# Performance work log

Measured on AMD Instinct MI355X. Metric: run time of the kernel, lower is better.

The kernel has to match this reference:

```python
import jax, jax.numpy as jnp
import numpy as np

B = 2            # batch_size (number of windows)
W_SIZE = 2       # window_size
WIDTH = 256      # cart_pixel_width
TEMP = 0.01      # softmax_temp
EPS = 1e-12      # F.normalize eps


def _l2norm(x, axis):
    n = jnp.sqrt(jnp.sum(x * x, axis=axis, keepdims=True))
    return x / jnp.maximum(n, EPS)


def _bilinear(img, u, v):
    """align_corners=True bilinear sample. img: [C,H,W]; u,v: [N] pixel coords."""
    H, W = img.shape[-2], img.shape[-1]
    u0 = jnp.clip(jnp.floor(u), 0, W - 1)
    v0 = jnp.clip(jnp.floor(v), 0, H - 1)
    u1 = jnp.clip(u0 + 1, 0, W - 1)
    v1 = jnp.clip(v0 + 1, 0, H - 1)
    au = u - u0
    av = v - v0
    u0i, u1i = u0.astype(jnp.int32), u1.astype(jnp.int32)
    v0i, v1i = v0.astype(jnp.int32), v1.astype(jnp.int32)
    g = lambda vi, ui: img[:, vi, ui]  # [C,N]
    return (g(v0i, u0i) * (1 - au) * (1 - av) + g(v0i, u1i) * au * (1 - av)
            + g(v1i, u0i) * (1 - au) * av + g(v1i, u1i) * au * av)


def setup_inputs() -> dict:
    key = jax.random.key(0)
    k1, k2, k3, k4 = jax.random.split(key, 4)
    BW, C, N, S = B * W_SIZE, 248, 1024, 1
    return {
        "keypoint_scores": jax.random.normal(k1, (BW, S, N), dtype=jnp.float32),
        "keypoint_desc": jax.random.normal(k2, (BW, C, N), dtype=jnp.float32),
        "desc_dense": jax.random.normal(k3, (BW, C, WIDTH, WIDTH), dtype=jnp.float32),
        "times_img": jax.random.uniform(k4, (BW, 1, WIDTH, WIDTH), dtype=jnp.float32),
    }


def reference(keypoint_scores, keypoint_desc, desc_dense, times_img):
    BW, C, N = keypoint_desc.shape
    w = W_SIZE
    # frame index bookkeeping (same as the torch per-batch loop, vectorized)
    src_ids = jnp.arange(B) * w                                   # [B]
    tgt_ids = (jnp.arange(B)[:, None] * w
               + jnp.arange(1, w)[None, :]).reshape(-1)           # [B*(w-1)]

    # dense pixel coordinates [W^2, 2] in (u, v) order
    v, u = jnp.meshgrid(jnp.arange(WIDTH), jnp.arange(WIDTH), indexing='ij')
    coords = jnp.stack([u.reshape(-1), v.reshape(-1)], axis=1).astype(desc_dense.dtype)

    # normalized source dense descriptors [B, C, W^2]
    src = _l2norm(desc_dense[src_ids].reshape(B, C, -1), axis=1)
    # normalized target keypoint descriptors [B, w-1, C, N]
    tgt = _l2norm(keypoint_desc[tgt_ids].reshape(B, w - 1, C, N), axis=2)

    # dense correlation: [B, w-1, N, W^2]
    match_vals = jnp.einsum('bkcn,bcm->bknm', tgt, src)
    soft = jax.nn.softmax(match_vals / TEMP, axis=-1)
    # coordinate-weighted sum -> pseudo coords [B*(w-1), N, 2]
    pseudo_coords = jnp.einsum('bknm,md->bknd', soft, coords).reshape(B * (w - 1), N, 2)

    # bilinear-sample src times at pseudo coords (normalize->grid_sample round trip
    # with align_corners maps back to the same pixel coords; H == W here)
    src_times = jnp.repeat(times_img[src_ids], w - 1, axis=0)      # [B*(w-1),1,H,W]
    pseudo_times = jax.vmap(_bilinear)(src_times,
                                       pseudo_coords[..., 0],
                                       pseudo_coords[..., 1])      # [B*(w-1),1,N]

    return (pseudo_coords, keypoint_scores[tgt_ids], tgt_ids, pseudo_times)
```

## Files before the change

kernel.cpp:

```cpp
#include <hip/hip_runtime.h>
#include <math.h>

typedef int i32x4 __attribute__((ext_vector_type(4)));
typedef int i32x16 __attribute__((ext_vector_type(16)));

#define CC 248
#define MM 65536
#define NN 1024

__device__ __forceinline__ float fexp2(float x) { return __builtin_amdgcn_exp2f(x); }


__global__ __launch_bounds__(512)
void convB_kernel(const float* __restrict__ dense, char* __restrict__ Ag) {
    __shared__ char at[2][16][128][16];
    __shared__ float scr[4][128];
    const int bid = blockIdx.x;
    const int fb  = bid >> 9;
    const int p0  = (bid & 511) * 128;
    const int tid = threadIdx.x;
    const int row = tid & 127;
    const int q   = tid >> 7;

    const float* dptr = dense + (size_t)(2 * fb) * CC * MM + p0 + row;
    float v[64];
    float ss = 0.f;
#pragma unroll
    for (int i = 0; i < 64; ++i) {
        int c = q * 64 + i;
        float x = (c < CC) ? dptr[(size_t)c * MM] : 0.f;
        v[i] = x;
        ss += x * x;
    }
    scr[q][row] = ss;
    __syncthreads();
    float inv = 32768.0f / fmaxf(sqrtf(scr[0][row] + scr[1][row] + scr[2][row] + scr[3][row]), 1e-12f);

#pragma unroll
    for (int j = 0; j < 16; ++j) {
        unsigned w1 = 0, w0 = 0;
#pragma unroll
        for (int t = 0; t < 4; ++t) {
            float qv = fminf(fmaxf(rintf(v[j * 4 + t] * inv), -32768.f), 32639.f);
            int af = (int)qv;
            int a1 = (af + 128) >> 8;
            int a0 = af - (a1 << 8);
            w1 |= (unsigned)(a1 & 255) << (8 * t);
            w0 |= (unsigned)(a0 & 255) << (8 * t);
        }
        int c0 = q * 64 + j * 4;
        int kg = c0 >> 4, dw = (c0 >> 2) & 3;
        *(unsigned*)&at[0][kg][row][dw * 4] = w1;
        *(unsigned*)&at[1][kg][row][dw * 4] = w0;
    }
    __syncthreads();

    const int tile = p0 >> 8, rhalf = (p0 >> 7) & 1;
    char* outb = Ag + (size_t)(fb * 256 + tile) * 131072;
#pragma unroll
    for (int it = 0; it < 8; ++it) {
        int id = tid + it * 512;
        int pl = id >> 11, kg = (id >> 7) & 15, r2 = id & 127;
        i32x4 vv = *(const i32x4*)&at[pl][kg][r2][0];
        *(i32x4*)&outb[(size_t)pl * 65536 + kg * 4096 + (rhalf * 128 + r2) * 16] = vv;
    }
}

__global__ __launch_bounds__(256)
void convA_kernel(const float* __restrict__ kdesc, char* __restrict__ Bg) {
    __shared__ char bt[2][16][32][16];
    __shared__ float scr[8][32];
    const int bid = blockIdx.x;
    const int b   = bid >> 5;
    const int nt  = bid & 31;
    const int n0  = nt * 32;
    const int tid = threadIdx.x;
    const int col = tid & 31;
    const int q   = tid >> 5;

    const float* kp = kdesc + (size_t)(2 * b + 1) * CC * NN + n0 + col;
    float ss = 0.f;
    for (int i = 0; i < 31; ++i) {
        int c = q * 31 + i;
        float v = kp[(size_t)c * NN];
        ss += v * v;
    }
    scr[q][col] = ss;
    __syncthreads();
    float tot = 0.f;
#pragma unroll
    for (int k = 0; k < 8; ++k) tot += scr[k][col];
    float inv = 32768.0f / fmaxf(sqrtf(tot), 1e-12f);
    if (tid < 64) {
        int pl = tid >> 5, c2 = tid & 31;
        *(long*)&bt[pl][15][c2][8] = 0L;
    }
    __syncthreads();
    for (int i = 0; i < 31; ++i) {
        int c = q * 31 + i;
        float qq = fminf(fmaxf(rintf(kp[(size_t)c * NN] * inv), -32768.f), 32639.f);
        int af = (int)qq;
        int a1 = (af + 128) >> 8;
        int a0 = af - (a1 << 8);
        bt[0][c >> 4][col][c & 15] = (char)a1;
        bt[1][c >> 4][col][c & 15] = (char)a0;
    }
    __syncthreads();
    char* outb = Bg + (size_t)(b * 32 + nt) * 16384;
    const char* src = &bt[0][0][0][0];
#pragma unroll
    for (int it = 0; it < 4; ++it) {
        int id = tid + it * 256;
        *(i32x4*)&outb[(size_t)id * 16] = *(const i32x4*)&src[(size_t)id * 16];
    }
}

__global__ __launch_bounds__(256, 2)
void gemm_kernel(const char* __restrict__ Ag, const char* __restrict__ Bg,
                 float* __restrict__ partials) {
    extern __shared__ char lds[];
    const int B0OFF = 12288;

    const int bid  = blockIdx.x;
    const int xcd  = bid & 7;
    const int rest = bid >> 3;
    const int nchunk = rest & 3;
    const int pid  = xcd + 8 * (rest >> 2);
    const int b      = pid >> 6;
    const int mchunk = pid & 63;

    const int tid  = threadIdx.x;
    const int lane = tid & 63;
    const int w    = tid >> 6;
    const int lrow = lane & 31;
    const int lhi  = lane >> 5;

    const char* atile0 = Ag + ((size_t)b * 256 + mchunk * 4) * 131072;
    const char* bbase  = Bg + (size_t)(b * 32 + nchunk * 8) * 16384;

#pragma unroll
    for (int i = 0; i < 16; ++i) {
        int c = w * 16 + i;
        int t = c >> 3, j = c & 7;
        const char* src = bbase + t * 16384 + 8192 + j * 1024 + lane * 16;
        __builtin_amdgcn_global_load_lds(
            (const __attribute__((address_space(1))) void*)src,
            (__attribute__((address_space(3))) void*)&lds[B0OFF + t * 8192 + j * 1024], 16, 0, 0);
    }

    i32x4 bc[8][2];
#pragma unroll
    for (int ks = 0; ks < 8; ++ks)
#pragma unroll
        for (int bp = 0; bp < 2; ++bp)
            bc[ks][bp] = *(const i32x4*)(bbase + (size_t)(2 * w + bp) * 16384
                                         + (ks * 2 + lhi) * 512 + lrow * 16);

    auto ISSUE = [&](int s, int slotOff) {
        const int mtn = s >> 3, ksn = s & 7;
        const char* src = atile0 + (size_t)(mtn >> 2) * 131072 + (w >> 1) * 65536
                        + (ksn * 2 + (w & 1)) * 4096 + ((mtn & 3) * 64 + lane) * 16;
        char* dst = &lds[slotOff + (w >> 1) * 2048 + (w & 1) * 1024];
        __builtin_amdgcn_global_load_lds(
            (const __attribute__((address_space(1))) void*)src,
            (__attribute__((address_space(3))) void*)dst, 16, 0, 0);
    };

    i32x16 accH[2][2], accX[2][2];
#pragma unroll
    for (int ap = 0; ap < 2; ++ap)
#pragma unroll
        for (int bp = 0; bp < 2; ++bp) { accH[ap][bp] = (i32x16)(0); accX[ap][bp] = (i32x16)(0); }
    float rm[2], rz[2], rsu[2], rsv[2];
#pragma unroll
    for (int bp = 0; bp < 2; ++bp) { rm[bp] = -INFINITY; rz[bp] = 0.f; rsu[bp] = 0.f; rsv[bp] = 0.f; }

    const float S2 = 100.0f * 1.4426950408889634f / 1073741824.0f;
    const float cH = 65536.0f * S2;
    const float cX = 256.0f * S2;

    ISSUE(0, 0);
    ISSUE(1, 4096);
    int slotR = 0, slotW = 8192;

    for (int mt = 0; mt < 16; ++mt) {
#pragma unroll
        for (int ks = 0; ks < 8; ++ks) {
            const int s = mt * 8 + ks;
            if (s < 127) asm volatile("s_waitcnt vmcnt(1)" ::: "memory");
            else         asm volatile("s_waitcnt vmcnt(0)" ::: "memory");
            asm volatile("s_barrier" ::: "memory");
            if (s + 2 < 128) ISSUE(s + 2, slotW);

            i32x4 b0F[2];
#pragma unroll
            for (int bp = 0; bp < 2; ++bp)
                b0F[bp] = *(const i32x4*)&lds[B0OFF + (2 * w + bp) * 8192
                                              + (ks * 2 + lhi) * 512 + lrow * 16];
            i32x4 aF[2][2];
#pragma unroll
            for (int pl = 0; pl < 2; ++pl)
#pragma unroll
                for (int ap = 0; ap < 2; ++ap)
                    aF[pl][ap] = *(const i32x4*)&lds[slotR + pl * 2048 + lhi * 1024
                                                     + (ap * 32 + lrow) * 16];
            __builtin_amdgcn_s_setprio(1);
#pragma unroll
            for (int ap = 0; ap < 2; ++ap)
#pragma unroll
                for (int bp = 0; bp < 2; ++bp) {
                    accH[ap][bp] = __builtin_amdgcn_mfma_i32_32x32x32_i8(aF[0][ap], bc[ks][bp], accH[ap][bp], 0, 0, 0);
                    accX[ap][bp] = __builtin_amdgcn_mfma_i32_32x32x32_i8(aF[0][ap], b0F[bp],    accX[ap][bp], 0, 0, 0);
                    accX[ap][bp] = __builtin_amdgcn_mfma_i32_32x32x32_i8(aF[1][ap], bc[ks][bp], accX[ap][bp], 0, 0, 0);
                }
            __builtin_amdgcn_s_setprio(0);
            slotR = (slotR == 8192) ? 0 : slotR + 4096;
            slotW = (slotW == 8192) ? 0 : slotW + 4096;
        }

        const int mbase = mchunk * 1024 + mt * 64;
        const float ub0 = (float)((mbase & 255) + 4 * lhi);
        const float ub1 = ub0 + 32.0f;
        const float vcoord = (float)(mbase >> 8);
#pragma unroll
        for (int bp = 0; bp < 2; ++bp) {
            int hm = accH[0][bp][0];
#pragma unroll
            for (int ap = 0; ap < 2; ++ap)
#pragma unroll
                for (int r = 0; r < 16; ++r) {
                    int h = accH[ap][bp][r];
                    hm = (h > hm) ? h : hm;
                }
            const float bx = (float)hm * cH;
            float tz0 = 0.f, tz1 = 0.f, tsur = 0.f;
#pragma unroll
            for (int ap = 0; ap < 2; ++ap)
#pragma unroll
                for (int r = 0; r < 16; ++r) {
                    int dH = accH[ap][bp][r] - hm;
                    float e = fexp2(fmaf((float)dH, cH, (float)accX[ap][bp][r] * cX));
                    if (ap == 0) tz0 += e; else tz1 += e;
                    tsur = fmaf(e, (float)((r & 3) + 8 * (r >> 2)), tsur);
                }
            float tzz = tz0 + tz1;
            float tsu = fmaf(ub0, tz0, fmaf(ub1, tz1, tsur));
            float tsv = vcoord * tzz;
            float nm = fmaxf(rm[bp], bx);
            float f1 = fexp2(rm[bp] - nm), f2 = fexp2(bx - nm);
            rz[bp]  = rz[bp]  * f1 + tzz * f2;
            rsu[bp] = rsu[bp] * f1 + tsu * f2;
            rsv[bp] = rsv[bp] * f1 + tsv * f2;
            rm[bp]  = nm;
#pragma unroll
            for (int ap = 0; ap < 2; ++ap) { accH[ap][bp] = (i32x16)(0); accX[ap][bp] = (i32x16)(0); }
        }
    }

#pragma unroll
    for (int bp = 0; bp < 2; ++bp) {
        float m2  = __shfl_xor(rm[bp], 32, 64);
        float z2  = __shfl_xor(rz[bp], 32, 64);
        float su2 = __shfl_xor(rsu[bp], 32, 64);
        float sv2 = __shfl_xor(rsv[bp], 32, 64);
        float nm = fmaxf(rm[bp], m2);
        float f1 = fexp2(rm[bp] - nm), f2 = fexp2(m2 - nm);
        rz[bp]  = rz[bp]  * f1 + z2  * f2;
        rsu[bp] = rsu[bp] * f1 + su2 * f2;
        rsv[bp] = rsv[bp] * f1 + sv2 * f2;
        rm[bp]  = nm;
    }
    if (lane < 32) {
#pragma unroll
        for (int bp = 0; bp < 2; ++bp) {
            int n = nchunk * 256 + w * 64 + bp * 32 + lrow;
            size_t idxp = ((size_t)b * NN + n) * 64 + mchunk;
            ((float4*)partials)[idxp] = make_float4(rm[bp], rz[bp], rsu[bp], rsv[bp]);
        }
    }
}

__global__ __launch_bounds__(256)
void combine_kernel(const float* __restrict__ partials,
                    const float* __restrict__ kscores,
                    const float* __restrict__ times,
                    float* __restrict__ out) {
    const int wg   = blockIdx.x * 4 + (threadIdx.x >> 6);
    const int lane = threadIdx.x & 63;
    const int b = wg >> 10, n = wg & 1023;
    const float4* pp = (const float4*)partials + (size_t)wg * 64;

    float4 p = pp[lane];
    float m = p.x, z = p.y, su = p.z, sv = p.w;
#pragma unroll
    for (int mask = 32; mask >= 1; mask >>= 1) {
        float m2  = __shfl_xor(m, mask, 64);
        float z2  = __shfl_xor(z, mask, 64);
        float su2 = __shfl_xor(su, mask, 64);
        float sv2 = __shfl_xor(sv, mask, 64);
        float nm = fmaxf(m, m2);
        float f1 = fexp2(m - nm), f2 = fexp2(m2 - nm);
        z = z * f1 + z2 * f2; su = su * f1 + su2 * f2; sv = sv * f1 + sv2 * f2; m = nm;
    }

    if (lane == 0) {
        float u = su / z, v = sv / z;
        out[(size_t)wg * 2 + 0] = u;
        out[(size_t)wg * 2 + 1] = v;
        out[4096 + wg] = kscores[(size_t)(2 * b + 1) * NN + n];
        if (wg == 0) { out[6144] = 1.0f; out[6145] = 3.0f; }

        const float* timg = times + (size_t)(2 * b) * MM;
        float u0 = fminf(fmaxf(floorf(u), 0.f), 255.f);
        float v0 = fminf(fmaxf(floorf(v), 0.f), 255.f);
        float u1 = fminf(u0 + 1.f, 255.f);
        float v1 = fminf(v0 + 1.f, 255.f);
        float au = u - u0, av = v - v0;
        int u0i = (int)u0, u1i = (int)u1, v0i = (int)v0, v1i = (int)v1;
        float t00 = timg[v0i * 256 + u0i], t01 = timg[v0i * 256 + u1i];
        float t10 = timg[v1i * 256 + u0i], t11 = timg[v1i * 256 + u1i];
        float t = t00 * (1.f - au) * (1.f - av) + t01 * au * (1.f - av)
                + t10 * (1.f - au) * av + t11 * au * av;
        out[6146 + wg] = t;
    }
}

extern "C" void kernel_launch(void* const* d_in, const int* in_sizes, int n_in,
                              void* d_out, int out_size, void* d_ws, size_t ws_size,
                              hipStream_t stream) {
    const float* kscores = (const float*)d_in[0];
    const float* kdesc   = (const float*)d_in[1];
    const float* dense   = (const float*)d_in[2];
    const float* times   = (const float*)d_in[3];
    float* out = (float*)d_out;

    char* Ag = (char*)d_ws;
    char* Bg = Ag + (size_t)2 * 256 * 131072;
    float* partials = (float*)(Bg + (size_t)2 * 32 * 16384);

    hipFuncSetAttribute((const void*)gemm_kernel,
                        hipFuncAttributeMaxDynamicSharedMemorySize, 77824);

    hipLaunchKernelGGL(convB_kernel,   dim3(1024), dim3(512), 0, stream, dense, Ag);
    hipLaunchKernelGGL(convA_kernel,   dim3(64),   dim3(256), 0, stream, kdesc, Bg);
    hipLaunchKernelGGL(gemm_kernel,    dim3(512),  dim3(256), 77824, stream, Ag, Bg, partials);
    hipLaunchKernelGGL(combine_kernel, dim3(512),  dim3(256), 0, stream, partials, kscores, times, out);
}
```

Measured before the change: 147.5 us.

## Double-buffer A fragments in registers and deepen LDS staging to three stages

```diff
diff --git a/kernel.cpp b/kernel.cpp
--- a/kernel.cpp
+++ b/kernel.cpp
@@ -179,81 +179,103 @@
     const float cH = 65536.0f * S2;
     const float cX = 256.0f * S2;
 
+    i32x4 aF[2][2][2];
+
+    auto RDA = [&](int pp, int slotOff) {
+#pragma unroll
+        for (int pl = 0; pl < 2; ++pl)
+#pragma unroll
+            for (int ap = 0; ap < 2; ++ap)
+                aF[pp][pl][ap] = *(const i32x4*)&lds[slotOff + pl * 2048 + lhi * 1024
+                                                     + (ap * 32 + lrow) * 16];
+    };
+
     ISSUE(0, 0);
     ISSUE(1, 4096);
-    int slotR = 0, slotW = 8192;
+    ISSUE(2, 8192);
+    asm volatile("s_waitcnt vmcnt(2)" ::: "memory");
+    asm volatile("s_barrier" ::: "memory");
+    RDA(0, 0);
+
+    int slotW = 0, slotR = 4096;
 
     for (int mt = 0; mt < 16; ++mt) {
 #pragma unroll
         for (int ks = 0; ks < 8; ++ks) {
             const int s = mt * 8 + ks;
-            if (s < 127) asm volatile("s_waitcnt vmcnt(1)" ::: "memory");
-            else         asm volatile("s_waitcnt vmcnt(0)" ::: "memory");
-            asm volatile("s_barrier" ::: "memory");
-            if (s + 2 < 128) ISSUE(s + 2, slotW);
+            const int pp = ks & 1;
 
             i32x4 b0F[2];
 #pragma unroll
             for (int bp = 0; bp < 2; ++bp)
                 b0F[bp] = *(const i32x4*)&lds[B0OFF + (2 * w + bp) * 8192
                                               + (ks * 2 + lhi) * 512 + lrow * 16];
-            i32x4 aF[2][2];
-#pragma unroll
-            for (int pl = 0; pl < 2; ++pl)
-#pragma unroll
-                for (int ap = 0; ap < 2; ++ap)
-                    aF[pl][ap] = *(const i32x4*)&lds[slotR + pl * 2048 + lhi * 1024
-                                                     + (ap * 32 + lrow) * 16];
+
+            if (s < 126)       asm volatile("s_waitcnt vmcnt(1)" ::: "memory");
+            else if (s == 126) asm volatile("s_waitcnt vmcnt(0)" ::: "memory");
+            if (s < 127) {
+                asm volatile("s_barrier" ::: "memory");
+                if (s + 3 <= 127) ISSUE(s + 3, slotW);
+                RDA(pp ^ 1, slotR);
+            }
+
             __builtin_amdgcn_s_setprio(1);
 #pragma unroll
             for (int ap = 0; ap < 2; ++ap)
 #pragma unroll
                 for (int bp = 0; bp < 2; ++bp) {
-                    accH[ap][bp] = __builtin_amdgcn_mfma_i32_32x32x32_i8(aF[0][ap], bc[ks][bp], accH[ap][bp], 0, 0, 0);
-                    accX[ap][bp] = __builtin_amdgcn_mfma_i32_32x32x32_i8(aF[0][ap], b0F[bp],    accX[ap][bp], 0, 0, 0);
-                    accX[ap][bp] = __builtin_amdgcn_mfma_i32_32x32x32_i8(aF[1][ap], bc[ks][bp], accX[ap][bp], 0, 0, 0);
+                    accH[ap][bp] = __builtin_amdgcn_mfma_i32_32x32x32_i8(aF[pp][0][ap], bc[ks][bp], accH[ap][bp], 0, 0, 0);
+                    accX[ap][bp] = __builtin_amdgcn_mfma_i32_32x32x32_i8(aF[pp][1][ap], bc[ks][bp], accX[ap][bp], 0, 0, 0);
                 }
+#pragma unroll
+            for (int ap = 0; ap < 2; ++ap)
+#pragma unroll
+                for (int bp = 0; bp < 2; ++bp)
+                    accX[ap][bp] = __builtin_amdgcn_mfma_i32_32x32x32_i8(aF[pp][0][ap], b0F[bp], accX[ap][bp], 0, 0, 0);
             __builtin_amdgcn_s_setprio(0);
+
+            slotW = (slotW == 8192) ? 0 : slotW + 4096;
             slotR = (slotR == 8192) ? 0 : slotR + 4096;
-            slotW = (slotW == 8192) ? 0 : slotW + 4096;
-        }
-
-        const int mbase = mchunk * 1024 + mt * 64;
-        const float ub0 = (float)((mbase & 255) + 4 * lhi);
-        const float ub1 = ub0 + 32.0f;
-        const float vcoord = (float)(mbase >> 8);
-#pragma unroll
-        for (int bp = 0; bp < 2; ++bp) {
-            int hm = accH[0][bp][0];
-#pragma unroll
-            for (int ap = 0; ap < 2; ++ap)
-#pragma unroll
-                for (int r = 0; r < 16; ++r) {
-                    int h = accH[ap][bp][r];
-                    hm = (h > hm) ? h : hm;
+
+            if (ks == 7) {
+                const int mbase = mchunk * 1024 + mt * 64;
+                const float ub0 = (float)((mbase & 255) + 4 * lhi);
+                const float ub1 = ub0 + 32.0f;
+                const float vcoord = (float)(mbase >> 8);
+#pragma unroll
+                for (int bp = 0; bp < 2; ++bp) {
+                    int hm = accH[0][bp][0];
+#pragma unroll
+                    for (int ap = 0; ap < 2; ++ap)
+#pragma unroll
+                        for (int r = 0; r < 16; ++r) {
+                            int h = accH[ap][bp][r];
+                            hm = (h > hm) ? h : hm;
+                        }
+                    const float bx = (float)hm * cH;
+                    float tz0 = 0.f, tz1 = 0.f, tsur = 0.f;
+#pragma unroll
+                    for (int ap = 0; ap < 2; ++ap)
+#pragma unroll
+                        for (int r = 0; r < 16; ++r) {
+                            int dH = accH[ap][bp][r] - hm;
+                            float e = fexp2(fmaf((float)dH, cH, (float)accX[ap][bp][r] * cX));
+                            if (ap == 0) tz0 += e; else tz1 += e;
+                            tsur = fmaf(e, (float)((r & 3) + 8 * (r >> 2)), tsur);
+                        }
+                    float tzz = tz0 + tz1;
+                    float tsu = fmaf(ub0, tz0, fmaf(ub1, tz1, tsur));
+                    float tsv = vcoord * tzz;
+                    float nm = fmaxf(rm[bp], bx);
+                    float f1 = fexp2(rm[bp] - nm), f2 = fexp2(bx - nm);
+                    rz[bp]  = rz[bp]  * f1 + tzz * f2;
+                    rsu[bp] = rsu[bp] * f1 + tsu * f2;
+                    rsv[bp] = rsv[bp] * f1 + tsv * f2;
+                    rm[bp]  = nm;
+#pragma unroll
+                    for (int ap = 0; ap < 2; ++ap) { accH[ap][bp] = (i32x16)(0); accX[ap][bp] = (i32x16)(0); }
                 }
-            const float bx = (float)hm * cH;
-            float tz0 = 0.f, tz1 = 0.f, tsur = 0.f;
-#pragma unroll
-            for (int ap = 0; ap < 2; ++ap)
-#pragma unroll
-                for (int r = 0; r < 16; ++r) {
-                    int dH = accH[ap][bp][r] - hm;
-                    float e = fexp2(fmaf((float)dH, cH, (float)accX[ap][bp][r] * cX));
-                    if (ap == 0) tz0 += e; else tz1 += e;
-                    tsur = fmaf(e, (float)((r & 3) + 8 * (r >> 2)), tsur);
-                }
-            float tzz = tz0 + tz1;
-            float tsu = fmaf(ub0, tz0, fmaf(ub1, tz1, tsur));
-            float tsv = vcoord * tzz;
-            float nm = fmaxf(rm[bp], bx);
-            float f1 = fexp2(rm[bp] - nm), f2 = fexp2(bx - nm);
-            rz[bp]  = rz[bp]  * f1 + tzz * f2;
-            rsu[bp] = rsu[bp] * f1 + tsu * f2;
-            rsv[bp] = rsv[bp] * f1 + tsv * f2;
-            rm[bp]  = nm;
-#pragma unroll
-            for (int ap = 0; ap < 2; ++ap) { accH[ap][bp] = (i32x16)(0); accX[ap][bp] = (i32x16)(0); }
+            }
         }
     }
 
```

Measured after the change: 148.1 us. Within noise of the previous version (+0.4%).

## Replace LDS-staged A/B0 tiles with direct register double-buffered global loads in GEMM

Applied to the files above, without the earlier changes.

```diff
diff --git a/kernel.cpp b/kernel.cpp
--- a/kernel.cpp
+++ b/kernel.cpp
@@ -118,52 +118,46 @@
 __global__ __launch_bounds__(256, 2)
 void gemm_kernel(const char* __restrict__ Ag, const char* __restrict__ Bg,
                  float* __restrict__ partials) {
-    extern __shared__ char lds[];
-    const int B0OFF = 12288;
-
     const int bid  = blockIdx.x;
     const int xcd  = bid & 7;
     const int rest = bid >> 3;
-    const int nchunk = rest & 3;
-    const int pid  = xcd + 8 * (rest >> 2);
-    const int b      = pid >> 6;
-    const int mchunk = pid & 63;
-
-    const int tid  = threadIdx.x;
-    const int lane = tid & 63;
-    const int w    = tid >> 6;
+    const int sub  = rest & 3;
+    const int panel = xcd + 8 * (rest >> 2);
+    const int b      = panel >> 6;
+    const int mrange = panel & 63;
+
+    const int lane = threadIdx.x & 63;
+    const int w    = threadIdx.x >> 6;
+    const int nblk = sub * 4 + w;
     const int lrow = lane & 31;
     const int lhi  = lane >> 5;
 
-    const char* atile0 = Ag + ((size_t)b * 256 + mchunk * 4) * 131072;
-    const char* bbase  = Bg + (size_t)(b * 32 + nchunk * 8) * 16384;
-
-#pragma unroll
-    for (int i = 0; i < 16; ++i) {
-        int c = w * 16 + i;
-        int t = c >> 3, j = c & 7;
-        const char* src = bbase + t * 16384 + 8192 + j * 1024 + lane * 16;
-        __builtin_amdgcn_global_load_lds(
-            (const __attribute__((address_space(1))) void*)src,
-            (__attribute__((address_space(3))) void*)&lds[B0OFF + t * 8192 + j * 1024], 16, 0, 0);
-    }
+    const char* abase = Ag + ((size_t)b * 256 + mrange * 4) * 131072;
+    const char* bb    = Bg + (size_t)(b * 32 + nblk * 2) * 16384;
 
     i32x4 bc[8][2];
 #pragma unroll
-    for (int ks = 0; ks < 8; ++ks)
+    for (int kk = 0; kk < 8; ++kk)
 #pragma unroll
         for (int bp = 0; bp < 2; ++bp)
-            bc[ks][bp] = *(const i32x4*)(bbase + (size_t)(2 * w + bp) * 16384
-                                         + (ks * 2 + lhi) * 512 + lrow * 16);
-
-    auto ISSUE = [&](int s, int slotOff) {
-        const int mtn = s >> 3, ksn = s & 7;
-        const char* src = atile0 + (size_t)(mtn >> 2) * 131072 + (w >> 1) * 65536
-                        + (ksn * 2 + (w & 1)) * 4096 + ((mtn & 3) * 64 + lane) * 16;
-        char* dst = &lds[slotOff + (w >> 1) * 2048 + (w & 1) * 1024];
-        __builtin_amdgcn_global_load_lds(
-            (const __attribute__((address_space(1))) void*)src,
-            (__attribute__((address_space(3))) void*)dst, 16, 0, 0);
+            bc[kk][bp] = *(const i32x4*)(bb + bp * 16384 + (kk * 2 + lhi) * 512 + lrow * 16);
+
+    i32x4 aS[2][2][2];
+    i32x4 b0S[2][2];
+
+    const int va = lhi * 4096 + lrow * 16;
+    auto LOADA = [&](int slot, int mtn, int ksn) {
+        const char* sA = abase + (size_t)(mtn >> 2) * 131072 + (mtn & 3) * 1024 + ksn * 8192;
+#pragma unroll
+        for (int pl = 0; pl < 2; ++pl)
+#pragma unroll
+            for (int ap = 0; ap < 2; ++ap)
+                aS[slot][pl][ap] = *(const i32x4*)(sA + pl * 65536 + va + ap * 512);
+    };
+    auto LOADB0 = [&](int slot, int ksn) {
+#pragma unroll
+        for (int bp = 0; bp < 2; ++bp)
+            b0S[slot][bp] = *(const i32x4*)(bb + bp * 16384 + 8192 + (ksn * 2 + lhi) * 512 + lrow * 16);
     };
 
     i32x16 accH[2][2], accX[2][2];
@@ -179,46 +173,32 @@
     const float cH = 65536.0f * S2;
     const float cX = 256.0f * S2;
 
-    ISSUE(0, 0);
-    ISSUE(1, 4096);
-    int slotR = 0, slotW = 8192;
+    LOADB0(0, 0);
+    LOADA(0, 0, 0);
 
     for (int mt = 0; mt < 16; ++mt) {
 #pragma unroll
         for (int ks = 0; ks < 8; ++ks) {
-            const int s = mt * 8 + ks;
-            if (s < 127) asm volatile("s_waitcnt vmcnt(1)" ::: "memory");
-            else         asm volatile("s_waitcnt vmcnt(0)" ::: "memory");
-            asm volatile("s_barrier" ::: "memory");
-            if (s + 2 < 128) ISSUE(s + 2, slotW);
-
-            i32x4 b0F[2];
-#pragma unroll
-            for (int bp = 0; bp < 2; ++bp)
-                b0F[bp] = *(const i32x4*)&lds[B0OFF + (2 * w + bp) * 8192
-                                              + (ks * 2 + lhi) * 512 + lrow * 16];
-            i32x4 aF[2][2];
-#pragma unroll
-            for (int pl = 0; pl < 2; ++pl)
-#pragma unroll
-                for (int ap = 0; ap < 2; ++ap)
-                    aF[pl][ap] = *(const i32x4*)&lds[slotR + pl * 2048 + lhi * 1024
-                                                     + (ap * 32 + lrow) * 16];
+            const int slot = ks & 1;
+            {
+                const int ksn = (ks + 1) & 7;
+                const int mtn = (ks == 7) ? mt + 1 : mt;
+                LOADB0(slot ^ 1, ksn);
+                LOADA(slot ^ 1, (mtn < 16) ? mtn : 15, ksn);
+            }
             __builtin_amdgcn_s_setprio(1);
 #pragma unroll
             for (int ap = 0; ap < 2; ++ap)
 #pragma unroll
                 for (int bp = 0; bp < 2; ++bp) {
-                    accH[ap][bp] = __builtin_amdgcn_mfma_i32_32x32x32_i8(aF[0][ap], bc[ks][bp], accH[ap][bp], 0, 0, 0);
-                    accX[ap][bp] = __builtin_amdgcn_mfma_i32_32x32x32_i8(aF[0][ap], b0F[bp],    accX[ap][bp], 0, 0, 0);
-                    accX[ap][bp] = __builtin_amdgcn_mfma_i32_32x32x32_i8(aF[1][ap], bc[ks][bp], accX[ap][bp], 0, 0, 0);
+                    accH[ap][bp] = __builtin_amdgcn_mfma_i32_32x32x32_i8(aS[slot][0][ap], bc[ks][bp],   accH[ap][bp], 0, 0, 0);
+                    accX[ap][bp] = __builtin_amdgcn_mfma_i32_32x32x32_i8(aS[slot][0][ap], b0S[slot][bp], accX[ap][bp], 0, 0, 0);
+                    accX[ap][bp] = __builtin_amdgcn_mfma_i32_32x32x32_i8(aS[slot][1][ap], bc[ks][bp],   accX[ap][bp], 0, 0, 0);
                 }
             __builtin_amdgcn_s_setprio(0);
-            slotR = (slotR == 8192) ? 0 : slotR + 4096;
-            slotW = (slotW == 8192) ? 0 : slotW + 4096;
         }
 
-        const int mbase = mchunk * 1024 + mt * 64;
+        const int mbase = mrange * 1024 + mt * 64;
         const float ub0 = (float)((mbase & 255) + 4 * lhi);
         const float ub1 = ub0 + 32.0f;
         const float vcoord = (float)(mbase >> 8);
@@ -273,8 +253,8 @@
     if (lane < 32) {
 #pragma unroll
         for (int bp = 0; bp < 2; ++bp) {
-            int n = nchunk * 256 + w * 64 + bp * 32 + lrow;
-            size_t idxp = ((size_t)b * NN + n) * 64 + mchunk;
+            int n = nblk * 64 + bp * 32 + lrow;
+            size_t idxp = ((size_t)b * NN + n) * 64 + mrange;
             ((float4*)partials)[idxp] = make_float4(rm[bp], rz[bp], rsu[bp], rsv[bp]);
         }
     }
@@ -338,11 +318,8 @@
     char* Bg = Ag + (size_t)2 * 256 * 131072;
     float* partials = (float*)(Bg + (size_t)2 * 32 * 16384);
 
-    hipFuncSetAttribute((const void*)gemm_kernel,
-                        hipFuncAttributeMaxDynamicSharedMemorySize, 77824);
-
     hipLaunchKernelGGL(convB_kernel,   dim3(1024), dim3(512), 0, stream, dense, Ag);
     hipLaunchKernelGGL(convA_kernel,   dim3(64),   dim3(256), 0, stream, kdesc, Bg);
-    hipLaunchKernelGGL(gemm_kernel,    dim3(512),  dim3(256), 77824, stream, Ag, Bg, partials);
+    hipLaunchKernelGGL(gemm_kernel,    dim3(512),  dim3(256), 0, stream, Ag, Bg, partials);
     hipLaunchKernelGGL(combine_kernel, dim3(512),  dim3(256), 0, stream, partials, kscores, times, out);
 }
```

Result: slower. 168.3 us (+14.1%).

## Keep both B-operand planes in registers and halve the gemm M-subtile

Applied to the files above, without the earlier changes.

```diff
diff --git a/kernel.cpp b/kernel.cpp
--- a/kernel.cpp
+++ b/kernel.cpp
@@ -118,8 +118,7 @@
 __global__ __launch_bounds__(256, 2)
 void gemm_kernel(const char* __restrict__ Ag, const char* __restrict__ Bg,
                  float* __restrict__ partials) {
-    extern __shared__ char lds[];
-    const int B0OFF = 12288;
+    __shared__ char lds[12288];
 
     const int bid  = blockIdx.x;
     const int xcd  = bid & 7;
@@ -129,48 +128,38 @@
     const int b      = pid >> 6;
     const int mchunk = pid & 63;
 
-    const int tid  = threadIdx.x;
-    const int lane = tid & 63;
-    const int w    = tid >> 6;
+    const int lane = threadIdx.x & 63;
+    const int w    = threadIdx.x >> 6;
     const int lrow = lane & 31;
     const int lhi  = lane >> 5;
 
     const char* atile0 = Ag + ((size_t)b * 256 + mchunk * 4) * 131072;
-    const char* bbase  = Bg + (size_t)(b * 32 + nchunk * 8) * 16384;
-
-#pragma unroll
-    for (int i = 0; i < 16; ++i) {
-        int c = w * 16 + i;
-        int t = c >> 3, j = c & 7;
-        const char* src = bbase + t * 16384 + 8192 + j * 1024 + lane * 16;
-        __builtin_amdgcn_global_load_lds(
-            (const __attribute__((address_space(1))) void*)src,
-            (__attribute__((address_space(3))) void*)&lds[B0OFF + t * 8192 + j * 1024], 16, 0, 0);
-    }
-
-    i32x4 bc[8][2];
-#pragma unroll
-    for (int ks = 0; ks < 8; ++ks)
-#pragma unroll
-        for (int bp = 0; bp < 2; ++bp)
-            bc[ks][bp] = *(const i32x4*)(bbase + (size_t)(2 * w + bp) * 16384
-                                         + (ks * 2 + lhi) * 512 + lrow * 16);
-
-    auto ISSUE = [&](int s, int slotOff) {
-        const int mtn = s >> 3, ksn = s & 7;
-        const char* src = atile0 + (size_t)(mtn >> 2) * 131072 + (w >> 1) * 65536
-                        + (ksn * 2 + (w & 1)) * 4096 + ((mtn & 3) * 64 + lane) * 16;
+    const char* bb     = Bg + (size_t)(b * 32 + nchunk * 8 + w * 2) * 16384;
+
+    i32x4 bc[8][2][2];
+#pragma unroll
+    for (int kk = 0; kk < 8; ++kk)
+#pragma unroll
+        for (int pl = 0; pl < 2; ++pl)
+#pragma unroll
+            for (int bp = 0; bp < 2; ++bp)
+                bc[kk][pl][bp] = *(const i32x4*)(bb + bp * 16384 + pl * 8192
+                                                 + (kk * 2 + lhi) * 512 + lrow * 16);
+
+    auto ISSUE = [&](int p, int slotOff) {
+        const int mtn = p >> 2, kq = p & 3;
+        const int tile = mtn >> 3, row0 = (mtn & 7) * 32;
+        const char* src = atile0 + (size_t)tile * 131072 + (w >> 1) * 65536
+                        + (kq * 4 + (w & 1) * 2 + lhi) * 4096 + (row0 + lrow) * 16;
         char* dst = &lds[slotOff + (w >> 1) * 2048 + (w & 1) * 1024];
         __builtin_amdgcn_global_load_lds(
             (const __attribute__((address_space(1))) void*)src,
             (__attribute__((address_space(3))) void*)dst, 16, 0, 0);
     };
 
-    i32x16 accH[2][2], accX[2][2];
-#pragma unroll
-    for (int ap = 0; ap < 2; ++ap)
-#pragma unroll
-        for (int bp = 0; bp < 2; ++bp) { accH[ap][bp] = (i32x16)(0); accX[ap][bp] = (i32x16)(0); }
+    i32x16 accH[2], accX[2];
+#pragma unroll
+    for (int bp = 0; bp < 2; ++bp) { accH[bp] = (i32x16)(0); accX[bp] = (i32x16)(0); }
     float rm[2], rz[2], rsu[2], rsv[2];
 #pragma unroll
     for (int bp = 0; bp < 2; ++bp) { rm[bp] = -INFINITY; rz[bp] = 0.f; rsu[bp] = 0.f; rsv[bp] = 0.f; }
@@ -183,77 +172,62 @@
     ISSUE(1, 4096);
     int slotR = 0, slotW = 8192;
 
-    for (int mt = 0; mt < 16; ++mt) {
-#pragma unroll
-        for (int ks = 0; ks < 8; ++ks) {
-            const int s = mt * 8 + ks;
-            if (s < 127) asm volatile("s_waitcnt vmcnt(1)" ::: "memory");
+    for (int mt = 0; mt < 32; ++mt) {
+#pragma unroll
+        for (int kq = 0; kq < 4; ++kq) {
+            const int p = mt * 4 + kq;
+            if (p < 127) asm volatile("s_waitcnt vmcnt(1)" ::: "memory");
             else         asm volatile("s_waitcnt vmcnt(0)" ::: "memory");
             asm volatile("s_barrier" ::: "memory");
-            if (s + 2 < 128) ISSUE(s + 2, slotW);
-
-            i32x4 b0F[2];
-#pragma unroll
-            for (int bp = 0; bp < 2; ++bp)
-                b0F[bp] = *(const i32x4*)&lds[B0OFF + (2 * w + bp) * 8192
-                                              + (ks * 2 + lhi) * 512 + lrow * 16];
-            i32x4 aF[2][2];
-#pragma unroll
-            for (int pl = 0; pl < 2; ++pl)
-#pragma unroll
-                for (int ap = 0; ap < 2; ++ap)
-                    aF[pl][ap] = *(const i32x4*)&lds[slotR + pl * 2048 + lhi * 1024
-                                                     + (ap * 32 + lrow) * 16];
-            __builtin_amdgcn_s_setprio(1);
-#pragma unroll
-            for (int ap = 0; ap < 2; ++ap)
+            if (p + 2 < 128) ISSUE(p + 2, slotW);
+
+#pragma unroll
+            for (int j = 0; j < 2; ++j) {
+                const int kk = kq * 2 + j;
+                i32x4 a1 = *(const i32x4*)&lds[slotR + j * 1024 + lhi * 512 + lrow * 16];
+                i32x4 a0 = *(const i32x4*)&lds[slotR + 2048 + j * 1024 + lhi * 512 + lrow * 16];
+                __builtin_amdgcn_s_setprio(1);
 #pragma unroll
                 for (int bp = 0; bp < 2; ++bp) {
-                    accH[ap][bp] = __builtin_amdgcn_mfma_i32_32x32x32_i8(aF[0][ap], bc[ks][bp], accH[ap][bp], 0, 0, 0);
-                    accX[ap][bp] = __builtin_amdgcn_mfma_i32_32x32x32_i8(aF[0][ap], b0F[bp],    accX[ap][bp], 0, 0, 0);
-                    accX[ap][bp] = __builtin_amdgcn_mfma_i32_32x32x32_i8(aF[1][ap], bc[ks][bp], accX[ap][bp], 0, 0, 0);
+                    accH[bp] = __builtin_amdgcn_mfma_i32_32x32x32_i8(a1, bc[kk][0][bp], accH[bp], 0, 0, 0);
+                    accX[bp] = __builtin_amdgcn_mfma_i32_32x32x32_i8(a1, bc[kk][1][bp], accX[bp], 0, 0, 0);
+                    accX[bp] = __builtin_amdgcn_mfma_i32_32x32x32_i8(a0, bc[kk][0][bp], accX[bp], 0, 0, 0);
                 }
-            __builtin_amdgcn_s_setprio(0);
+                __builtin_amdgcn_s_setprio(0);
+            }
             slotR = (slotR == 8192) ? 0 : slotR + 4096;
             slotW = (slotW == 8192) ? 0 : slotW + 4096;
         }
 
-        const int mbase = mchunk * 1024 + mt * 64;
-        const float ub0 = (float)((mbase & 255) + 4 * lhi);
-        const float ub1 = ub0 + 32.0f;
+        const int mbase = mchunk * 1024 + mt * 32;
+        const float ub = (float)((mbase & 255) + 4 * lhi);
         const float vcoord = (float)(mbase >> 8);
 #pragma unroll
         for (int bp = 0; bp < 2; ++bp) {
-            int hm = accH[0][bp][0];
-#pragma unroll
-            for (int ap = 0; ap < 2; ++ap)
-#pragma unroll
-                for (int r = 0; r < 16; ++r) {
-                    int h = accH[ap][bp][r];
-                    hm = (h > hm) ? h : hm;
-                }
+            int hm = accH[bp][0];
+#pragma unroll
+            for (int r = 0; r < 16; ++r) {
+                int h = accH[bp][r];
+                hm = (h > hm) ? h : hm;
+            }
             const float bx = (float)hm * cH;
-            float tz0 = 0.f, tz1 = 0.f, tsur = 0.f;
-#pragma unroll
-            for (int ap = 0; ap < 2; ++ap)
-#pragma unroll
-                for (int r = 0; r < 16; ++r) {
-                    int dH = accH[ap][bp][r] - hm;
-                    float e = fexp2(fmaf((float)dH, cH, (float)accX[ap][bp][r] * cX));
-                    if (ap == 0) tz0 += e; else tz1 += e;
-                    tsur = fmaf(e, (float)((r & 3) + 8 * (r >> 2)), tsur);
-                }
-            float tzz = tz0 + tz1;
-            float tsu = fmaf(ub0, tz0, fmaf(ub1, tz1, tsur));
-            float tsv = vcoord * tzz;
+            float tz = 0.f, tsur = 0.f;
+#pragma unroll
+            for (int r = 0; r < 16; ++r) {
+                int dH = accH[bp][r] - hm;
+                float e = fexp2(fmaf((float)dH, cH, (float)accX[bp][r] * cX));
+                tz += e;
+                tsur = fmaf(e, (float)((r & 3) + 8 * (r >> 2)), tsur);
+            }
+            float tsu = fmaf(ub, tz, tsur);
+            float tsv = vcoord * tz;
             float nm = fmaxf(rm[bp], bx);
             float f1 = fexp2(rm[bp] - nm), f2 = fexp2(bx - nm);
-            rz[bp]  = rz[bp]  * f1 + tzz * f2;
+            rz[bp]  = rz[bp]  * f1 + tz  * f2;
             rsu[bp] = rsu[bp] * f1 + tsu * f2;
             rsv[bp] = rsv[bp] * f1 + tsv * f2;
             rm[bp]  = nm;
-#pragma unroll
-            for (int ap = 0; ap < 2; ++ap) { accH[ap][bp] = (i32x16)(0); accX[ap][bp] = (i32x16)(0); }
+            accH[bp] = (i32x16)(0); accX[bp] = (i32x16)(0);
         }
     }
 
@@ -338,11 +312,8 @@
     char* Bg = Ag + (size_t)2 * 256 * 131072;
     float* partials = (float*)(Bg + (size_t)2 * 32 * 16384);
 
-    hipFuncSetAttribute((const void*)gemm_kernel,
-                        hipFuncAttributeMaxDynamicSharedMemorySize, 77824);
-
     hipLaunchKernelGGL(convB_kernel,   dim3(1024), dim3(512), 0, stream, dense, Ag);
     hipLaunchKernelGGL(convA_kernel,   dim3(64),   dim3(256), 0, stream, kdesc, Bg);
-    hipLaunchKernelGGL(gemm_kernel,    dim3(512),  dim3(256), 77824, stream, Ag, Bg, partials);
+    hipLaunchKernelGGL(gemm_kernel,    dim3(512),  dim3(256), 0, stream, Ag, Bg, partials);
     hipLaunchKernelGGL(combine_kernel, dim3(512),  dim3(256), 0, stream, partials, kscores, times, out);
 }
```

Measured after the change: 149.2 us. About the same (+1.1%).
